# Kernel tuning notes

Measured on AMD Instinct MI355X. Metric: run time of the kernel, lower is better.

## Reference

```python
import jax, jax.numpy as jnp
import numpy as np

N = 576        # variable nodes (from filename wman_N0576)
MROWS = 144    # check nodes = N*(1 - 3/4)
ROW_DEG = 15   # check-node degree (WiMAX rate-3/4 style)
BATCH = 256
ITERS = 3


def _make_H():
    # deterministic binary parity-check matrix with fixed row degree >= 2
    rng = np.random.default_rng(0)
    cols = np.argsort(rng.random((MROWS, N)), axis=1)[:, :ROW_DEG]
    H = np.zeros((MROWS, N), dtype=np.float32)
    H[np.arange(MROWS)[:, None], cols] = 1.0
    return jnp.asarray(H)


def setup_inputs() -> dict:
    key = jax.random.key(0)
    r = jax.random.normal(key, (BATCH, N), dtype=jnp.float32)  # channel LLRs
    alpha = jnp.full((ITERS,), 0.7, dtype=jnp.float32)
    beta = jnp.full((ITERS,), 0.05, dtype=jnp.float32)
    return {"r": r, "H": _make_H(), "alpha": alpha, "beta": beta}


def _c_to_v(M, H, node_idx, alpha, beta):
    # min-sum check-to-variable messages with offset beta and scale alpha
    abs_M = jnp.abs(M)                                   # [B, MROWS, N]
    masked = jnp.where(H == 1.0, abs_M, jnp.inf)
    neg_top, idx = jax.lax.top_k(-masked, 2)             # two smallest per row
    min1 = -neg_top[..., 0:1]
    min2 = -neg_top[..., 1:2]
    idx1 = idx[..., 0:1]
    E_abs = jnp.where(node_idx == idx1, min2, min1)      # exclude-self min
    valid = jnp.where(H == 1.0, jnp.sign(M), 1.0)
    row_prod = jnp.prod(valid, axis=2, keepdims=True)    # total sign per check
    E_sign = row_prod * valid                            # exclude-self sign
    E = alpha * E_sign * jnp.maximum(0.0, E_abs - beta)
    return E * H


def reference(r, H, alpha, beta):
    node_idx = jnp.arange(N)[None, None, :]              # [1,1,N]
    M = H[None, :, :] * r[:, None, :]                    # initial v->c messages
    E = jnp.zeros_like(M)
    for it in range(ITERS):
        E = _c_to_v(M, H, node_idx, alpha[it], beta[it])
        sum_E = jnp.sum(E, axis=1, keepdims=True)        # [B,1,N]
        M = (r[:, None, :] + sum_E - E) * H[None, :, :]
    return r + jnp.sum(E, axis=1)                        # posterior LLRs [B,N]
```

## Files before the change

### kernel.cpp

```cpp
#include <hip/hip_runtime.h>

#define NVAR   576
#define NROW   144
#define DEG    15
#define NEDGE  (NROW * DEG)
#define NBATCH 256
#define NITER  3
#define NT     192
#define NWORD  9

__global__ void build_bits_kernel(const float* __restrict__ H,
                                  unsigned long long* __restrict__ bits) {
    int gid  = blockIdx.x * blockDim.x + threadIdx.x;
    int wid  = gid >> 6;
    int lane = gid & 63;
    if (wid >= NROW * NWORD) return;
    float h = H[wid * 64 + lane];
    unsigned long long m = __ballot(h != 0.0f);
    if (lane == 0) bits[wid] = m;
}

__launch_bounds__(NT, 1)
__global__ void ldpc_minsum_kernel(const float* __restrict__ r,
                                   const unsigned long long* __restrict__ bits,
                                   const float* __restrict__ alpha,
                                   const float* __restrict__ beta,
                                   float* __restrict__ out) {
    __shared__ float rs[NVAR];
    __shared__ float sA[NVAR];
    __shared__ float sB[NVAR];
    __shared__ short colsh[NROW * 16];

    const int b = blockIdx.x;
    const int t = threadIdx.x;

    float alr[NITER], ber[NITER];
    #pragma unroll
    for (int i = 0; i < NITER; ++i) { alr[i] = alpha[i]; ber[i] = beta[i]; }

    #pragma unroll
    for (int k = 0; k < 3; ++k) {
        int n = t + k * NT;
        rs[n] = r[b * NVAR + n];
        sA[n] = 0.0f;
    }

    if (t < NROW) {
        unsigned long long w[NWORD];
        #pragma unroll
        for (int i = 0; i < NWORD; ++i) w[i] = bits[t * NWORD + i];
        int k = 0;
        #pragma unroll
        for (int i = 0; i < NWORD; ++i) {
            unsigned long long bw = w[i];
            while (bw) {
                int p = __ffsll((long long)bw) - 1;
                bw &= bw - 1;
                colsh[t * 16 + k] = (short)(i * 64 + p);
                ++k;
            }
        }
    }
    __syncthreads();

    int   ci[DEG];
    float Mv[DEG], Ev[DEG], rc[DEG];
    if (t < NROW) {
        #pragma unroll
        for (int j = 0; j < DEG; ++j) ci[j] = (int)colsh[t * 16 + j];
        #pragma unroll
        for (int j = 0; j < DEG; ++j) { rc[j] = rs[ci[j]]; Mv[j] = rc[j]; }
    }

    #pragma unroll
    for (int it = 0; it < NITER; ++it) {
        float* sum = (it & 1) ? sB : sA;
        float* nxt = (it & 1) ? sA : sB;

        if (t < NROW) {
            float m1 = INFINITY, m2 = INFINITY, sg = 1.0f;
            int j1 = 0;
            #pragma unroll
            for (int j = 0; j < DEG; ++j) {
                float v = Mv[j];
                float a = fabsf(v);
                float s = (v > 0.0f) ? 1.0f : ((v < 0.0f) ? -1.0f : 0.0f);
                sg *= s;
                if (a < m1) { m2 = m1; m1 = a; j1 = j; }
                else if (a < m2) { m2 = a; }
            }
            #pragma unroll
            for (int j = 0; j < DEG; ++j) {
                float v = Mv[j];
                float s = (v > 0.0f) ? 1.0f : ((v < 0.0f) ? -1.0f : 0.0f);
                float eabs = (j == j1) ? m2 : m1;
                float e = alr[it] * sg * s * fmaxf(0.0f, eabs - ber[it]);
                Ev[j] = e;
                atomicAdd(&sum[ci[j]], e);
            }
        }
        __syncthreads();

        if (it == NITER - 1) {
            #pragma unroll
            for (int k = 0; k < 3; ++k) {
                int n = t + k * NT;
                out[b * NVAR + n] = rs[n] + sum[n];
            }
        } else {
            #pragma unroll
            for (int k = 0; k < 3; ++k) nxt[t + k * NT] = 0.0f;
            if (t < NROW) {
                #pragma unroll
                for (int j = 0; j < DEG; ++j)
                    Mv[j] = rc[j] + sum[ci[j]] - Ev[j];
            }
            __syncthreads();
        }
    }
}

extern "C" void kernel_launch(void* const* d_in, const int* in_sizes, int n_in,
                              void* d_out, int out_size, void* d_ws, size_t ws_size,
                              hipStream_t stream) {
    const float* r     = (const float*)d_in[0];
    const float* H     = (const float*)d_in[1];
    const float* alpha = (const float*)d_in[2];
    const float* beta  = (const float*)d_in[3];
    float* out = (float*)d_out;
    unsigned long long* bits = (unsigned long long*)d_ws;

    build_bits_kernel<<<(NROW * NWORD * 64 + 255) / 256, 256, 0, stream>>>(H, bits);
    ldpc_minsum_kernel<<<NBATCH, NT, 0, stream>>>(r, bits, alpha, beta, out);
}
```

Measured before the change: 75.00 us.

## Replace LDS atomic scatter with CSC gather of per-edge messages

Adds a single-block kernel that builds, from the H bitmask, a column-to-edge index list (CSC) and the per-row column lists. The decode kernel then stores check-to-variable messages per edge in LDS and sums each variable by gathering through the CSC indices, replacing shared-memory atomicAdd scatter and the per-iteration zeroing of double-buffered sum arrays. This adds a third kernel launch and a serial 144-row loop in the CSC builder. Column degree is capped at 16, and any edge past that cap is silently dropped, which would give wrong sums for heavier columns.

```diff
diff --git a/kernel.cpp b/kernel.cpp
--- a/kernel.cpp
+++ b/kernel.cpp
@@ -1,35 +1,74 @@
 #include <hip/hip_runtime.h>
 
-#define NVAR   576
-#define NROW   144
-#define DEG    15
-#define NEDGE  (NROW * DEG)
-#define NBATCH 256
-#define NITER  3
-#define NT     192
-#define NWORD  9
+#define NVAR    576
+#define NROW    144
+#define DEG     15
+#define NITER   3
+#define NWORD   9
+#define NWTOT   (NROW * NWORD)
+#define MAXD    16
+#define ESTRIDE 17
+#define EZERO   (143 * ESTRIDE + DEG - 1 + 1)
+#define ESIZE   (EZERO + 2)
+#define NT      192
 
 __global__ void build_bits_kernel(const float* __restrict__ H,
                                   unsigned long long* __restrict__ bits) {
     int gid  = blockIdx.x * blockDim.x + threadIdx.x;
     int wid  = gid >> 6;
     int lane = gid & 63;
-    if (wid >= NROW * NWORD) return;
+    if (wid >= NWTOT) return;
     float h = H[wid * 64 + lane];
     unsigned long long m = __ballot(h != 0.0f);
     if (lane == 0) bits[wid] = m;
 }
 
+__launch_bounds__(576, 1)
+__global__ void build_csc_kernel(const unsigned long long* __restrict__ bits,
+                                 unsigned short* __restrict__ cols_rows,
+                                 unsigned short* __restrict__ csc) {
+    __shared__ unsigned long long bitw[NWTOT];
+    __shared__ int pf[NROW * NWORD];
+
+    const int t = threadIdx.x;
+    for (int i = t; i < NWTOT; i += 576) bitw[i] = bits[i];
+    __syncthreads();
+
+    if (t < NROW) {
+        int acc = 0;
+        #pragma unroll
+        for (int w = 0; w < NWORD; ++w) {
+            pf[t * NWORD + w] = acc;
+            acc += __popcll(bitw[t * NWORD + w]);
+        }
+    }
+    __syncthreads();
+
+    const int wsel = t >> 6, bitpos = t & 63;
+    int deg = 0;
+    for (int m = 0; m < NROW; ++m) {
+        unsigned long long word = bitw[m * NWORD + wsel];
+        if ((word >> bitpos) & 1ull) {
+            int j = pf[m * NWORD + wsel]
+                  + (int)__popcll(word & ((1ull << bitpos) - 1ull));
+            if (deg < MAXD) csc[t * MAXD + deg] = (unsigned short)(m * ESTRIDE + j);
+            ++deg;
+            cols_rows[m * 16 + j] = (unsigned short)t;
+        }
+    }
+    for (int d = deg; d < MAXD; ++d) csc[t * MAXD + d] = (unsigned short)EZERO;
+}
+
 __launch_bounds__(NT, 1)
-__global__ void ldpc_minsum_kernel(const float* __restrict__ r,
-                                   const unsigned long long* __restrict__ bits,
+__global__ void ldpc_decode_kernel(const float* __restrict__ r,
+                                   const unsigned short* __restrict__ cols_rows,
+                                   const unsigned short* __restrict__ csc,
                                    const float* __restrict__ alpha,
                                    const float* __restrict__ beta,
                                    float* __restrict__ out) {
     __shared__ float rs[NVAR];
-    __shared__ float sA[NVAR];
-    __shared__ float sB[NVAR];
-    __shared__ short colsh[NROW * 16];
+    __shared__ float Elds[ESIZE];
+    __shared__ float sumE[NVAR];
 
     const int b = blockIdx.x;
     const int t = threadIdx.x;
@@ -39,44 +78,37 @@
     for (int i = 0; i < NITER; ++i) { alr[i] = alpha[i]; ber[i] = beta[i]; }
 
     #pragma unroll
+    for (int k = 0; k < 3; ++k) rs[t + k * NT] = r[b * NVAR + t + k * NT];
+    if (t == 0) { Elds[EZERO] = 0.0f; Elds[EZERO + 1] = 0.0f; }
+
+    unsigned int cw[3][8];
+    #pragma unroll
     for (int k = 0; k < 3; ++k) {
-        int n = t + k * NT;
-        rs[n] = r[b * NVAR + n];
-        sA[n] = 0.0f;
+        const uint4* p = (const uint4*)(csc + (t + k * NT) * MAXD);
+        uint4 a = p[0], c = p[1];
+        cw[k][0] = a.x; cw[k][1] = a.y; cw[k][2] = a.z; cw[k][3] = a.w;
+        cw[k][4] = c.x; cw[k][5] = c.y; cw[k][6] = c.z; cw[k][7] = c.w;
     }
 
+    int ci[DEG];
     if (t < NROW) {
-        unsigned long long w[NWORD];
+        const uint4* p = (const uint4*)(cols_rows + t * 16);
+        uint4 a = p[0], c = p[1];
+        unsigned int uw[8] = {a.x, a.y, a.z, a.w, c.x, c.y, c.z, c.w};
         #pragma unroll
-        for (int i = 0; i < NWORD; ++i) w[i] = bits[t * NWORD + i];
-        int k = 0;
-        #pragma unroll
-        for (int i = 0; i < NWORD; ++i) {
-            unsigned long long bw = w[i];
-            while (bw) {
-                int p = __ffsll((long long)bw) - 1;
-                bw &= bw - 1;
-                colsh[t * 16 + k] = (short)(i * 64 + p);
-                ++k;
-            }
-        }
+        for (int j = 0; j < DEG; ++j)
+            ci[j] = (int)((uw[j >> 1] >> ((j & 1) * 16)) & 0xffffu);
     }
     __syncthreads();
 
-    int   ci[DEG];
     float Mv[DEG], Ev[DEG], rc[DEG];
     if (t < NROW) {
-        #pragma unroll
-        for (int j = 0; j < DEG; ++j) ci[j] = (int)colsh[t * 16 + j];
         #pragma unroll
         for (int j = 0; j < DEG; ++j) { rc[j] = rs[ci[j]]; Mv[j] = rc[j]; }
     }
 
     #pragma unroll
     for (int it = 0; it < NITER; ++it) {
-        float* sum = (it & 1) ? sB : sA;
-        float* nxt = (it & 1) ? sA : sB;
-
         if (t < NROW) {
             float m1 = INFINITY, m2 = INFINITY, sg = 1.0f;
             int j1 = 0;
@@ -96,26 +128,29 @@
                 float eabs = (j == j1) ? m2 : m1;
                 float e = alr[it] * sg * s * fmaxf(0.0f, eabs - ber[it]);
                 Ev[j] = e;
-                atomicAdd(&sum[ci[j]], e);
+                Elds[t * ESTRIDE + j] = e;
             }
         }
         __syncthreads();
 
-        if (it == NITER - 1) {
+        #pragma unroll
+        for (int k = 0; k < 3; ++k) {
+            float s = 0.0f;
             #pragma unroll
-            for (int k = 0; k < 3; ++k) {
-                int n = t + k * NT;
-                out[b * NVAR + n] = rs[n] + sum[n];
-            }
-        } else {
-            #pragma unroll
-            for (int k = 0; k < 3; ++k) nxt[t + k * NT] = 0.0f;
+            for (int d = 0; d < MAXD; ++d)
+                s += Elds[(cw[k][d >> 1] >> ((d & 1) * 16)) & 0xffffu];
+            int n = t + k * NT;
+            if (it == NITER - 1) out[b * NVAR + n] = rs[n] + s;
+            else                 sumE[n] = s;
+        }
+
+        if (it < NITER - 1) {
+            __syncthreads();
             if (t < NROW) {
                 #pragma unroll
                 for (int j = 0; j < DEG; ++j)
-                    Mv[j] = rc[j] + sum[ci[j]] - Ev[j];
+                    Mv[j] = rc[j] + sumE[ci[j]] - Ev[j];
             }
-            __syncthreads();
         }
     }
 }
@@ -128,8 +163,12 @@
     const float* alpha = (const float*)d_in[2];
     const float* beta  = (const float*)d_in[3];
     float* out = (float*)d_out;
-    unsigned long long* bits = (unsigned long long*)d_ws;
 
-    build_bits_kernel<<<(NROW * NWORD * 64 + 255) / 256, 256, 0, stream>>>(H, bits);
-    ldpc_minsum_kernel<<<NBATCH, NT, 0, stream>>>(r, bits, alpha, beta, out);
+    unsigned long long* bits      = (unsigned long long*)d_ws;
+    unsigned short*     cols_rows = (unsigned short*)((char*)d_ws + 10368);
+    unsigned short*     csc       = (unsigned short*)((char*)d_ws + 14976);
+
+    build_bits_kernel<<<(NWTOT * 64 + 255) / 256, 256, 0, stream>>>(H, bits);
+    build_csc_kernel<<<1, 576, 0, stream>>>(bits, cols_rows, csc);
+    ldpc_decode_kernel<<<256, NT, 0, stream>>>(r, cols_rows, csc, alpha, beta, out);
 }
```

Result: slower. 86.66 us (+15.5%).
